# Kernel optimization log

Measured on AMD Instinct MI355X. Metric: run time of the kernel, lower is better.

The kernel has to match this reference:

```python
import jax, jax.numpy as jnp
import numpy as np

R = 16      # grid resolution per axis (G = R**3 voxels)
K = 8       # num KNN neighbors per voxel
H = 64      # num_hidden
NB = 2      # num conv blocks
EPS = 1e-5


def _conv3d(x, w, b):
    # x: [B,C,D,H,W], w: [O,I,3,3,3]
    y = jax.lax.conv_general_dilated(
        x, w, window_strides=(1, 1, 1), padding='SAME',
        dimension_numbers=('NCDHW', 'OIDHW', 'NCDHW'))
    return y + b[None, :, None, None, None]


def _bn(x):
    # training-mode BatchNorm3d statistics (no affine), per channel
    m = x.mean(axis=(0, 2, 3, 4), keepdims=True)
    v = x.var(axis=(0, 2, 3, 4), keepdims=True)
    return (x - m) * jax.lax.rsqrt(v + EPS)


def _forward(pos, x, pe_w1, pe_b1, pe_w2, pe_b2, f_w, f_b, up_w, up_b,
             conv_w, conv_b, on_g, on_b, ro_w, ro_b):
    B, N, _ = pos.shape
    # ---- Gridifier: coordinate grid over domain [-1, 1]^3 ----
    g1 = jnp.linspace(-1.0, 1.0, R, dtype=pos.dtype)
    grid = jnp.stack(jnp.meshgrid(g1, g1, g1, indexing='ij'), axis=-1).reshape(-1, 3)  # [G,3]
    # ---- brute-force KNN: points -> grid voxels (per graph) ----
    gn = jnp.sum(grid * grid, axis=-1)          # [G]
    pn = jnp.sum(pos * pos, axis=-1)            # [B,N]
    d = gn[None, :, None] + pn[:, None, :] - 2.0 * jnp.einsum('gc,bnc->bgn', grid, pos)  # [B,G,N]
    idx = jax.lax.top_k(jax.lax.stop_gradient(-d), K)[1]  # [B,G,K] nearest point indices
    b_ix = jnp.arange(B)[:, None, None]
    p_nb = pos[b_ix, idx]                       # [B,G,K,3] neighbor positions
    f_nb = x[b_ix, idx]                         # [B,G,K,Cin] neighbor features
    # ---- BipartiteConv: position-conditioned messages, mean aggregation ----
    rel = p_nb - grid[None, :, None, :]         # relative positions [B,G,K,3]
    pe = jax.nn.gelu(rel @ pe_w1 + pe_b1) @ pe_w2 + pe_b2   # position embed [B,G,K,H]
    msg = pe * (f_nb @ f_w + f_b)               # multiplicative conditioning [B,G,K,H]
    agg = msg.mean(axis=2)                      # [B,G,H]
    h = jax.nn.gelu(agg @ up_w + up_b)          # update net [B,G,H]
    # reshape(B,R,R,R,H).permute(0,4,3,2,1) -> NCDHW
    vol = h.reshape(B, R, R, R, H).transpose(0, 4, 3, 2, 1)  # [B,H,R,R,R]
    # ---- ConvNet3D: residual blocks, maxpool after block 0 ----
    for i in range(NB):
        h1 = jax.nn.relu(_bn(_conv3d(vol, conv_w[i, 0], conv_b[i, 0])))
        h2 = _bn(_conv3d(h1, conv_w[i, 1], conv_b[i, 1]))
        vol = jax.nn.relu(vol + h2)
        if i == 0:
            vol = jax.lax.reduce_window(vol, -jnp.inf, jax.lax.max,
                                        (1, 1, 2, 2, 2), (1, 1, 2, 2, 2), 'VALID')
    out = _bn(vol) * on_g[None, :, None, None, None] + on_b[None, :, None, None, None]
    # ---- mean readout pool + linear head ----
    pooled = out.mean(axis=(2, 3, 4))           # [B,H]
    return pooled @ ro_w + ro_b                 # [B,out_channels]


def setup_inputs() -> dict:
    key = jax.random.key(0)
    ks = jax.random.split(key, 10)
    B, N, Cin, OUT = 4, 4096, 3, 16
    s = 0.05
    return {
        'pos': jax.random.uniform(ks[0], (B, N, 3), jnp.float32, -1.0, 1.0),
        'x': jax.random.normal(ks[1], (B, N, Cin), jnp.float32),
        'pe_w1': jax.random.normal(ks[2], (3, H), jnp.float32) * 0.3,
        'pe_b1': jnp.zeros((H,), jnp.float32),
        'pe_w2': jax.random.normal(ks[3], (H, H), jnp.float32) * s,
        'pe_b2': jnp.zeros((H,), jnp.float32),
        'f_w': jax.random.normal(ks[4], (Cin, H), jnp.float32) * 0.3,
        'f_b': jnp.zeros((H,), jnp.float32),
        'up_w': jax.random.normal(ks[5], (H, H), jnp.float32) * s,
        'up_b': jnp.zeros((H,), jnp.float32),
        'conv_w': jax.random.normal(ks[6], (NB, 2, H, H, 3, 3, 3), jnp.float32) * s,
        'conv_b': jnp.zeros((NB, 2, H), jnp.float32),
        'on_g': jnp.ones((H,), jnp.float32),
        'on_b': jnp.zeros((H,), jnp.float32),
        'ro_w': jax.random.normal(ks[7], (H, OUT), jnp.float32) * s,
        'ro_b': jnp.zeros((OUT,), jnp.float32),
    }


def reference(pos, x, pe_w1, pe_b1, pe_w2, pe_b2, f_w, f_b, up_w, up_b,
              conv_w, conv_b, on_g, on_b, ro_w, ro_b):
    return _forward(pos, x, pe_w1, pe_b1, pe_w2, pe_b2, f_w, f_b, up_w, up_b,
                    conv_w, conv_b, on_g, on_b, ro_w, ro_b)
```

## Files before the change

### kernel.cpp

```cpp
#include <hip/hip_runtime.h>

#define ULL unsigned long long
typedef unsigned short ush;
typedef __attribute__((ext_vector_type(8))) short s8v;
typedef __attribute__((ext_vector_type(4))) float f4v;

#define BB 4
#define NP 4096
#define HH 64
#define EPSF 1e-5f

#define WH_OFF      0u
#define WL_OFF      221184u
#define WT_PER_CONV 110592u
#define IDX_OFF     442368u
#define VOL0_OFF    573440u
#define V0H_OFF     2066432u
#define V0L_OFF     2812928u
#define T1_OFF      3559424u
#define VOL1_OFF    4608000u
#define V1H_OFF     4864000u
#define V1L_OFF     4992000u
#define T3_OFF      5120000u
#define STATS_OFF   5251072u
#define CELLS_OFF   5251968u
#define SPOS_OFF    5268368u
#define MW_OFF      5333904u

#define ZN_V0   373248u
#define ZN_V1   64000u
#define ZN_ST   224u
#define ZN_ALL  (ZN_V0 + ZN_V1 + ZN_ST)

__device__ __forceinline__ ush f2bf(float f) {
  unsigned u = __float_as_uint(f);
  return (ush)((u + 0x7FFFu + ((u >> 16) & 1u)) >> 16);
}
__device__ __forceinline__ float bf2f(ush h) { return __uint_as_float(((unsigned)h) << 16); }

__device__ __forceinline__ float gelu_tanh(float v) {
  float inner = 0.7978845608028654f * (v + 0.044715f * v * v * v);
  return 0.5f * v * (1.0f + tanhf(inner));
}

__device__ __forceinline__ float lin16(int i) {
  return -1.0f + (float)i * (2.0f / 15.0f);
}

__global__ __launch_bounds__(256) void k_prep(const float* __restrict__ cw,
                                              const float* __restrict__ pw2,
                                              const float* __restrict__ upw,
                                              ush* __restrict__ wh,
                                              ush* __restrict__ wl,
                                              ush* __restrict__ mw,
                                              float* __restrict__ ws) {
  unsigned i = blockIdx.x * 256u + threadIdx.x;
  float4 z = make_float4(0.f, 0.f, 0.f, 0.f);
  if (i < ZN_V0) ((float4*)(ws + V0H_OFF))[i] = z;
  else if (i < ZN_V0 + ZN_V1) ((float4*)(ws + V1H_OFF))[i - ZN_V0] = z;
  else if (i < ZN_ALL) ((float4*)(ws + STATS_OFF))[i - ZN_V0 - ZN_V1] = z;
  if (i < 442368u) {
    unsigned conv = i / WT_PER_CONV;
    unsigned r = i - conv * WT_PER_CONV;
    unsigned co = r / 1728u;
    unsigned r2 = r - co * 1728u;
    unsigned ci = r2 / 27u;
    unsigned off = r2 - ci * 27u;
    float w = cw[i];
    ush hi = f2bf(w);
    unsigned dst = conv * WT_PER_CONV + (off * 64u + co) * 64u + ci;
    wh[dst] = hi;
    wl[dst] = f2bf(w - bf2f(hi));
  } else if (i < 450560u) {
    unsigned t = i - 442368u;
    unsigned mat = t >> 12, r = t & 4095u;
    unsigned co = r >> 6, ci = r & 63u;
    const float* src = mat ? upw : pw2;
    float w = src[ci * 64u + co];
    ush hi = f2bf(w);
    mw[mat * 8192u + co * 64u + ci] = hi;
    mw[mat * 8192u + 4096u + co * 64u + ci] = f2bf(w - bf2f(hi));
  }
}

__global__ __launch_bounds__(256) void k_bin(const float* __restrict__ pos,
                                             int* __restrict__ cellStart,
                                             float4* __restrict__ sortedPos) {
  __shared__ int cnt[4096];
  __shared__ int wsum[4];
  int tid = threadIdx.x;
  int b = blockIdx.x;
  const float* pb = pos + b * NP * 3;
  for (int i = tid; i < 4096; i += 256) cnt[i] = 0;
  __syncthreads();
#pragma unroll
  for (int t = 0; t < 16; ++t) {
    int p = t * 256 + tid;
    float px = pb[3 * p], py = pb[3 * p + 1], pz = pb[3 * p + 2];
    int c0 = (int)floorf((px + 1.0f) * 7.5f + 0.5f);
    int c1 = (int)floorf((py + 1.0f) * 7.5f + 0.5f);
    int c2 = (int)floorf((pz + 1.0f) * 7.5f + 0.5f);
    c0 = min(max(c0, 0), 15); c1 = min(max(c1, 0), 15); c2 = min(max(c2, 0), 15);
    atomicAdd(&cnt[(c0 * 16 + c1) * 16 + c2], 1);
  }
  __syncthreads();
  int base = tid * 16;
  int loc[16];
  int run = 0;
#pragma unroll
  for (int j = 0; j < 16; ++j) { loc[j] = run; run += cnt[base + j]; }
  int lane = tid & 63, wv = tid >> 6;
  int inc = run;
  for (int d = 1; d < 64; d <<= 1) {
    int o = __shfl_up(inc, d, 64);
    if (lane >= d) inc += o;
  }
  if (lane == 63) wsum[wv] = inc;
  __syncthreads();
  int woff = 0;
  for (int w = 0; w < wv; ++w) woff += wsum[w];
  int excl = woff + inc - run;
  __syncthreads();
  int stv[16];
#pragma unroll
  for (int j = 0; j < 16; ++j) {
    stv[j] = excl + loc[j];
    cellStart[b * 4097 + base + j] = stv[j];
  }
#pragma unroll
  for (int j = 0; j < 16; ++j) cnt[base + j] = stv[j];
  if (tid == 0) cellStart[b * 4097 + 4096] = NP;
  __syncthreads();
#pragma unroll
  for (int t = 0; t < 16; ++t) {
    int p = t * 256 + tid;
    float px = pb[3 * p], py = pb[3 * p + 1], pz = pb[3 * p + 2];
    int c0 = (int)floorf((px + 1.0f) * 7.5f + 0.5f);
    int c1 = (int)floorf((py + 1.0f) * 7.5f + 0.5f);
    int c2 = (int)floorf((pz + 1.0f) * 7.5f + 0.5f);
    c0 = min(max(c0, 0), 15); c1 = min(max(c1, 0), 15); c2 = min(max(c2, 0), 15);
    int slot = atomicAdd(&cnt[(c0 * 16 + c1) * 16 + c2], 1);
    sortedPos[b * 4096 + slot] = make_float4(px, py, pz, __int_as_float(p));
  }
}

__device__ __forceinline__ void ins8(ULL* kk, ULL key) {
  if (key < kk[7]) {
    kk[7] = key;
#pragma unroll
    for (int q = 7; q >= 1; --q) {
      ULL a = kk[q - 1], c = kk[q];
      bool sw = c < a;
      kk[q - 1] = sw ? c : a;
      kk[q] = sw ? a : c;
    }
  }
}
__device__ __forceinline__ void merge4(ULL* kk, int sub, ULL& win0, ULL& win1) {
#pragma unroll
  for (int r = 0; r < 8; ++r) {
    ULL m = kk[0];
    ULL o = __shfl_xor(m, 1, 64); m = (o < m) ? o : m;
    o = __shfl_xor(m, 2, 64);     m = (o < m) ? o : m;
    if (kk[0] == m) {
#pragma unroll
      for (int q = 0; q < 7; ++q) kk[q] = kk[q + 1];
      kk[7] = ~0ULL;
    }
    if (sub == (r & 3)) { if (r < 4) win0 = m; else win1 = m; }
  }
}

__device__ __forceinline__ void scan_cell(const int* __restrict__ cs,
                                          const float4* __restrict__ sp,
                                          int cell, float gx, float gy, float gz,
                                          float gn, ULL* kk) {
  int st = cs[cell], en = cs[cell + 1];
  for (int p = st; p < en; ++p) {
    float4 c = sp[p];
    float pn = c.x * c.x + c.y * c.y + c.z * c.z;
    float dt = gx * c.x + gy * c.y + gz * c.z;
    float d = (gn + pn) - 2.0f * dt;
    unsigned u = __float_as_uint(d);
    u ^= (unsigned)((int)u >> 31) | 0x80000000u;
    ins8(kk, ((ULL)u << 32) | (unsigned)__float_as_uint(c.w));
  }
}

__global__ __launch_bounds__(256) void k_knn4(const int* __restrict__ cellStart,
                                              const float4* __restrict__ sortedPos,
                                              int* __restrict__ idxo) {
  constexpr int CAP = 3072;
  __shared__ float4 pts[CAP];
  __shared__ int rst[128], rlen[128], rof[128];
  __shared__ int Tsh;
  int tid = threadIdx.x;
  int lane = tid & 63;
  int sub = tid & 3;
  int lv = tid >> 2;
  int tile = blockIdx.x;
  int b = tile >> 6;
  int t6 = tile & 63;
  int ii0 = (t6 >> 4) * 4, jj0 = ((t6 >> 2) & 3) * 4, kk0 = (t6 & 3) * 4;
  int ii = ii0 + (lv >> 4), jj = jj0 + ((lv >> 2) & 3), kkc = kk0 + (lv & 3);
  int g = (ii << 8) | (jj << 4) | kkc;
  float gx = lin16(ii), gy = lin16(jj), gz = lin16(kkc);
  float gn = gx * gx + gy * gy + gz * gz;
  const int* cs = cellStart + b * 4097;
  const float4* sp = sortedPos + b * 4096;
  int loa = max(ii0 - 3, 0), hia = min(ii0 + 6, 15);
  int lob = max(jj0 - 3, 0), hib = min(jj0 + 6, 15);
  int loc = max(kk0 - 3, 0), hic = min(kk0 + 6, 15);
  int Ra = hia - loa + 1, Rb = hib - lob + 1;
  int nrows = Ra * Rb;
  if (tid < 128) {
    int st = 0, len = 0;
    if (tid < nrows) {
      int a = loa + tid / Rb, c1 = lob + tid % Rb;
      int base = (a * 16 + c1) * 16;
      st = cs[base + loc];
      len = cs[base + hic + 1] - st;
    }
    rst[tid] = st;
    rlen[tid] = len;
  }
  __syncthreads();
  if (tid < 64) {
    int l0v = rlen[lane], l1v = rlen[lane + 64];
    int s0 = l0v;
    for (int d = 1; d < 64; d <<= 1) { int o = __shfl_up(s0, d, 64); if (lane >= d) s0 += o; }
    int tot0 = __shfl(s0, 63, 64);
    int s1 = l1v;
    for (int d = 1; d < 64; d <<= 1) { int o = __shfl_up(s1, d, 64); if (lane >= d) s1 += o; }
    int tot1 = __shfl(s1, 63, 64);
    rof[lane] = s0 - l0v;
    rof[lane + 64] = tot0 + s1 - l1v;
    if (lane == 0) Tsh = tot0 + tot1;
  }
  __syncthreads();
  int T = Tsh;
  if (T <= CAP) {
    for (int i = tid; i < T; i += 256) {
      int lo = 0, hi = nrows - 1;
      while (lo < hi) { int mid = (lo + hi + 1) >> 1; if (rof[mid] <= i) lo = mid; else hi = mid - 1; }
      pts[i] = sp[rst[lo] + (i - rof[lo])];
    }
  }
  __syncthreads();
  ULL kk[8];
#pragma unroll
  for (int q = 0; q < 8; ++q) kk[q] = ~0ULL;
  if (T <= CAP) {
    for (int i = sub; i < T; i += 4) {
      float4 c = pts[i];
      float pn = c.x * c.x + c.y * c.y + c.z * c.z;
      float dt = gx * c.x + gy * c.y + gz * c.z;
      float d = (gn + pn) - 2.0f * dt;
      unsigned u = __float_as_uint(d);
      u ^= (unsigned)((int)u >> 31) | 0x80000000u;
      ins8(kk, ((ULL)u << 32) | (unsigned)__float_as_uint(c.w));
    }
  }
  ULL win0 = ~0ULL, win1 = ~0ULL;
  merge4(kk, sub, win0, win1);
  ULL w7 = __shfl(win1, lane | 3, 64);
  int dmin = 100;
  if (loa > 0)  dmin = min(dmin, ii - loa + 1);
  if (hia < 15) dmin = min(dmin, hia + 1 - ii);
  if (lob > 0)  dmin = min(dmin, jj - lob + 1);
  if (hib < 15) dmin = min(dmin, hib + 1 - jj);
  if (loc > 0)  dmin = min(dmin, kkc - loc + 1);
  if (hic < 15) dmin = min(dmin, hic + 1 - kkc);
  float bnd = ((float)dmin - 0.5f) * (2.0f / 15.0f) - 1e-5f;
  ULL ubk = ((ULL)(__float_as_uint(bnd * bnd) | 0x80000000u)) << 32;
  if (w7 >= ubk) {
#pragma unroll
    for (int q = 0; q < 8; ++q) kk[q] = ~0ULL;
    for (int t = sub; t < 1331; t += 4) {
      int dz = t / 121, r = t - dz * 121;
      int a = ii + dz - 5, c1 = jj + (r / 11) - 5, c2 = kkc + (r % 11) - 5;
      if (((unsigned)a > 15u) | ((unsigned)c1 > 15u) | ((unsigned)c2 > 15u)) continue;
      scan_cell(cs, sp, (a * 16 + c1) * 16 + c2, gx, gy, gz, gn, kk);
    }
    merge4(kk, sub, win0, win1);
    float bnd5 = 5.5f * (2.0f / 15.0f) - 1e-5f;
    ULL ub5 = ((ULL)(__float_as_uint(bnd5 * bnd5) | 0x80000000u)) << 32;
    w7 = __shfl(win1, lane | 3, 64);
    if (w7 >= ub5) {
#pragma unroll
      for (int q = 0; q < 8; ++q) kk[q] = ~0ULL;
      for (int p = sub; p < NP; p += 4) {
        float4 c = sp[p];
        float pn = c.x * c.x + c.y * c.y + c.z * c.z;
        float dt = gx * c.x + gy * c.y + gz * c.z;
        float d = (gn + pn) - 2.0f * dt;
        unsigned u = __float_as_uint(d);
        u ^= (unsigned)((int)u >> 31) | 0x80000000u;
        ins8(kk, ((ULL)u << 32) | (unsigned)__float_as_uint(c.w));
      }
      merge4(kk, sub, win0, win1);
    }
  }
  int addr = (((b << 12) | g) << 3);
  idxo[addr + sub] = (int)(win0 & 0xFFFFFFFFULL);
  idxo[addr + sub + 4] = (int)(win1 & 0xFFFFFFFFULL);
}

__global__ __launch_bounds__(256) void k_mlp2(
    const float* __restrict__ pos, const float* __restrict__ xf,
    const float* __restrict__ w1, const float* __restrict__ b1,
    const float* __restrict__ b2v, const float* __restrict__ fw,
    const float* __restrict__ fb, const float* __restrict__ ub,
    const ush* __restrict__ w2tH, const ush* __restrict__ w2tL,
    const ush* __restrict__ uwtH, const ush* __restrict__ uwtL,
    const int* __restrict__ idx, float* __restrict__ vol0,
    ush* __restrict__ v0h, ush* __restrict__ v0l) {
  __shared__ __align__(16) ush lhH[128 * 72];
  __shared__ __align__(16) ush lhL[128 * 72];
  __shared__ __align__(16) float lfe[128 * 68];
  __shared__ __align__(16) ush agH[16 * 72];
  __shared__ __align__(16) ush agL[16 * 72];
  __shared__ float gpb[128 * 8];
  int tid = threadIdx.x, lane = tid & 63, wv = tid >> 6;
  int lm = lane & 15, quad = lane >> 4;
  int b = blockIdx.x >> 8;
  int g0 = (blockIdx.x & 255) << 4;
  s8v BH[8], BL[8], UH[2], UL[2];
#pragma unroll
  for (int n = 0; n < 4; ++n)
#pragma unroll
    for (int ks = 0; ks < 2; ++ks) {
      int o = ((n * 16 + lm) << 6) + ks * 32 + (quad << 3);
      BH[n * 2 + ks] = *(const s8v*)(w2tH + o);
      BL[n * 2 + ks] = *(const s8v*)(w2tL + o);
    }
#pragma unroll
  for (int ks = 0; ks < 2; ++ks) {
    int o = ((wv * 16 + lm) << 6) + ks * 32 + (quad << 3);
    UH[ks] = *(const s8v*)(uwtH + o);
    UL[ks] = *(const s8v*)(uwtL + o);
  }
  if (tid < 128) {
    int vi = tid >> 3, kp = tid & 7;
    int g = g0 + vi;
    int p = idx[(((b << 12) | g) << 3) + kp];
    const float* pp = pos + (b * NP + p) * 3;
    const float* xp = xf + (b * NP + p) * 3;
    gpb[tid * 8 + 0] = pp[0]; gpb[tid * 8 + 1] = pp[1]; gpb[tid * 8 + 2] = pp[2];
    gpb[tid * 8 + 3] = xp[0]; gpb[tid * 8 + 4] = xp[1]; gpb[tid * 8 + 5] = xp[2];
  }
  float w10 = w1[lane], w11 = w1[64 + lane], w12 = w1[128 + lane], b1c = b1[lane];
  float fw0 = fw[lane], fw1 = fw[64 + lane], fw2 = fw[128 + lane], fbc = fb[lane];
  float ubc = ub[wv * 16 + lm];
  float gx = lin16(g0 >> 8), gy = lin16((g0 >> 4) & 15);
  __syncthreads();
  for (int i = 0; i < 32; ++i) {
    int pair = wv * 32 + i;
    int vi = pair >> 3;
    float gz = lin16(vi);
    float r0 = gpb[pair * 8 + 0] - gx, r1 = gpb[pair * 8 + 1] - gy, r2 = gpb[pair * 8 + 2] - gz;
    float h1 = gelu_tanh(fmaf(r2, w12, fmaf(r1, w11, fmaf(r0, w10, b1c))));
    float fe = fmaf(gpb[pair * 8 + 5], fw2,
                    fmaf(gpb[pair * 8 + 4], fw1, fmaf(gpb[pair * 8 + 3], fw0, fbc)));
    ush hi = f2bf(h1);
    lhH[pair * 72 + lane] = hi;
    lhL[pair * 72 + lane] = f2bf(h1 - bf2f(hi));
    lfe[pair * 68 + lane] = fe;
  }
  f4v acc[2][4];
#pragma unroll
  for (int m = 0; m < 2; ++m)
#pragma unroll
    for (int n = 0; n < 4; ++n) acc[m][n] = (f4v){0.f, 0.f, 0.f, 0.f};
#pragma unroll
  for (int m = 0; m < 2; ++m)
#pragma unroll
    for (int ks = 0; ks < 2; ++ks) {
      int ao = (wv * 32 + m * 16 + lm) * 72 + ks * 32 + quad * 8;
      s8v Ah = *(const s8v*)&lhH[ao];
      s8v Al = *(const s8v*)&lhL[ao];
#pragma unroll
      for (int n = 0; n < 4; ++n) {
        acc[m][n] = __builtin_amdgcn_mfma_f32_16x16x32_bf16(Ah, BH[n * 2 + ks], acc[m][n], 0, 0, 0);
        acc[m][n] = __builtin_amdgcn_mfma_f32_16x16x32_bf16(Ah, BL[n * 2 + ks], acc[m][n], 0, 0, 0);
        acc[m][n] = __builtin_amdgcn_mfma_f32_16x16x32_bf16(Al, BH[n * 2 + ks], acc[m][n], 0, 0, 0);
      }
    }
  float b2c[4];
#pragma unroll
  for (int n = 0; n < 4; ++n) b2c[n] = b2v[n * 16 + lm];
#pragma unroll
  for (int m = 0; m < 2; ++m) {
    int vox = wv * 4 + m * 2 + (quad >> 1);
#pragma unroll
    for (int n = 0; n < 4; ++n) {
      float s = 0.0f;
#pragma unroll
      for (int r = 0; r < 4; ++r) {
        int pair = wv * 32 + m * 16 + quad * 4 + r;
        s += (acc[m][n][r] + b2c[n]) * lfe[pair * 68 + n * 16 + lm];
      }
      s += __shfl_xor(s, 16, 64);
      s *= 0.125f;
      if ((quad & 1) == 0) {
        ush hi = f2bf(s);
        agH[vox * 72 + n * 16 + lm] = hi;
        agL[vox * 72 + n * 16 + lm] = f2bf(s - bf2f(hi));
      }
    }
  }
  __syncthreads();
  f4v a2 = (f4v){0.f, 0.f, 0.f, 0.f};
#pragma unroll
  for (int ks = 0; ks < 2; ++ks) {
    int ao = lm * 72 + ks * 32 + quad * 8;
    s8v Ah = *(const s8v*)&agH[ao];
    s8v Al = *(const s8v*)&agL[ao];
    a2 = __builtin_amdgcn_mfma_f32_16x16x32_bf16(Ah, UH[ks], a2, 0, 0, 0);
    a2 = __builtin_amdgcn_mfma_f32_16x16x32_bf16(Ah, UL[ks], a2, 0, 0, 0);
    a2 = __builtin_amdgcn_mfma_f32_16x16x32_bf16(Al, UH[ks], a2, 0, 0, 0);
  }
  int xc = g0 >> 8, yc = (g0 >> 4) & 15;
#pragma unroll
  for (int r = 0; r < 4; ++r) {
    int vox = quad * 4 + r;
    float h = gelu_tanh(a2[r] + ubc);
    int pidx = (((b * 18 + vox + 1) * 18 + yc + 1) * 18 + xc + 1) * 64 + wv * 16 + lm;
    vol0[pidx] = h;
    ush hi = f2bf(h);
    v0h[pidx] = hi;
    v0l[pidx] = f2bf(h - bf2f(hi));
  }
}

template <int Z>
__global__ __launch_bounds__(256) void k_convm(const ush* __restrict__ vh,
                                               const ush* __restrict__ vl,
                                               const ush* __restrict__ wh,
                                               const ush* __restrict__ wl,
                                               float* __restrict__ out,
                                               float* __restrict__ stats) {
  constexpr int P = Z + 2;
  constexpr int Py = (Z == 16) ? 6 : 10;
  constexpr int Px = (Z == 16) ? 18 : 10;
  constexpr int NV = 3 * Py * Px;
  constexpr int VS = 272;
  __shared__ unsigned char slab[NV * VS];
  __shared__ float ls[64], ls2[64];
  int tid = threadIdx.x;
  int lane = tid & 63, wv = tid >> 6;
  int vbase = blockIdx.x * 64;
  int b = (Z == 16) ? (vbase >> 12) : (vbase >> 9);
  int rem = vbase & (Z * Z * Z - 1);
  int z0 = rem / (Z * Z);
  int y0 = (Z == 16) ? ((rem & 255) >> 4) : 0;
  if (tid < 64) { ls[tid] = 0.0f; ls2[tid] = 0.0f; }
  {
    constexpr int NCH = NV * 8;
    for (int i = tid; i < NCH; i += 256) {
      int v = i >> 3, c = i & 7;
      int lz = v / (Py * Px);
      int r = v - lz * (Py * Px);
      int ly = r / Px, lx = r - ly * Px;
      int g = (((b * P + z0 + lz) * P + (y0 + ly)) * P + lx) * 64 + c * 8;
      *(uint4*)(slab + v * VS + c * 16)       = *(const uint4*)(vh + g);
      *(uint4*)(slab + v * VS + 128 + c * 16) = *(const uint4*)(vl + g);
    }
  }
  __syncthreads();
  int lm = lane & 15, quad = lane >> 4;
  int co = (wv << 4) | lm;
  f4v acc[4];
#pragma unroll
  for (int m = 0; m < 4; ++m) acc[m] = (f4v){0.f, 0.f, 0.f, 0.f};
  for (int off = 0; off < 27; ++off) {
    int dz = off / 9, r9 = off - dz * 9, dy = r9 / 3, dx = r9 - dy * 3;
    const ush* bph = wh + ((off * 64 + co) << 6) + (quad << 3);
    const ush* bpl = wl + ((off * 64 + co) << 6) + (quad << 3);
#pragma unroll
    for (int ks = 0; ks < 2; ++ks) {
      s8v bhf = *(const s8v*)(bph + ks * 32);
      s8v blf = *(const s8v*)(bpl + ks * 32);
#pragma unroll
      for (int m = 0; m < 4; ++m) {
        int lyp, lxp;
        if (Z == 16) { lyp = m + dy; lxp = lm + dx; }
        else         { lyp = 2 * m + (lm >> 3) + dy; lxp = (lm & 7) + dx; }
        int sv = (dz * Py + lyp) * Px + lxp;
        const unsigned char* ap = slab + sv * VS + (quad << 4) + (ks << 6);
        s8v ahf = *(const s8v*)(ap);
        s8v alf = *(const s8v*)(ap + 128);
        acc[m] = __builtin_amdgcn_mfma_f32_16x16x32_bf16(ahf, bhf, acc[m], 0, 0, 0);
        acc[m] = __builtin_amdgcn_mfma_f32_16x16x32_bf16(ahf, blf, acc[m], 0, 0, 0);
        acc[m] = __builtin_amdgcn_mfma_f32_16x16x32_bf16(alf, bhf, acc[m], 0, 0, 0);
      }
    }
  }
  float s = 0.0f, s2 = 0.0f;
#pragma unroll
  for (int m = 0; m < 4; ++m) {
    int vx = vbase + (m << 4) + (quad << 2);
#pragma unroll
    for (int r = 0; r < 4; ++r) {
      float v = acc[m][r];
      out[(vx + r) * 64 + co] = v;
      s += v;
      s2 = fmaf(v, v, s2);
    }
  }
  atomicAdd(&ls[co], s);
  atomicAdd(&ls2[co], s2);
  __syncthreads();
  if (tid < 64) {
    atomicAdd(&stats[tid * 2], ls[tid]);
    atomicAdd(&stats[tid * 2 + 1], ls2[tid]);
  }
}

template <int Z>
__global__ __launch_bounds__(256) void k_bnrelu(const float* __restrict__ t,
                                                const float* __restrict__ stats,
                                                ush* __restrict__ outh,
                                                ush* __restrict__ outl,
                                                float inv_cnt) {
  constexpr int P = Z + 2;
  unsigned i = blockIdx.x * 256u + threadIdx.x;
  int c = i & 63;
  int vox = i >> 6;
  int x = vox % Z;
  int q = vox / Z;
  int y = q % Z;
  q /= Z;
  int z = q % Z;
  int b = q / Z;
  float m = stats[c * 2] * inv_cnt;
  float var = stats[c * 2 + 1] * inv_cnt - m * m;
  float rs = 1.0f / sqrtf(var + EPSF);
  float v = (t[i] - m) * rs;
  v = v > 0.0f ? v : 0.0f;
  int pidx = (((b * P + z + 1) * P + y + 1) * P + x + 1) * 64 + c;
  ush hi = f2bf(v);
  outh[pidx] = hi;
  outl[pidx] = f2bf(v - bf2f(hi));
}

__global__ __launch_bounds__(256) void k_residpool(const float* __restrict__ vol0,
                                                   const float* __restrict__ t2,
                                                   const float* __restrict__ stats,
                                                   float* __restrict__ vol1,
                                                   ush* __restrict__ v1h,
                                                   ush* __restrict__ v1l) {
  unsigned i = blockIdx.x * 256u + threadIdx.x;
  int c = i & 63;
  int pv = i >> 6;
  int xp = pv & 7, yp = (pv >> 3) & 7, zp = (pv >> 6) & 7, b = pv >> 9;
  float m = stats[c * 2] * (1.0f / 16384.0f);
  float var = stats[c * 2 + 1] * (1.0f / 16384.0f) - m * m;
  float rs = 1.0f / sqrtf(var + EPSF);
  float best = 0.0f;
  for (int dz = 0; dz < 2; ++dz)
    for (int dy = 0; dy < 2; ++dy)
      for (int dx = 0; dx < 2; ++dx) {
        int z = 2 * zp + dz, y = 2 * yp + dy, x = 2 * xp + dx;
        float a = vol0[(((b * 18 + z + 1) * 18 + y + 1) * 18 + x + 1) * 64 + c];
        float t = t2[(b * 4096 + z * 256 + y * 16 + x) * 64 + c];
        float u = a + (t - m) * rs;
        u = u > 0.0f ? u : 0.0f;
        best = u > best ? u : best;
      }
  int pidx = (((b * 10 + zp + 1) * 10 + yp + 1) * 10 + xp + 1) * 64 + c;
  vol1[pidx] = best;
  ush hi = f2bf(best);
  v1h[pidx] = hi;
  v1l[pidx] = f2bf(best - bf2f(hi));
}

__global__ __launch_bounds__(256) void k_resid2(const float* __restrict__ vol1,
                                                const float* __restrict__ t4,
                                                const float* __restrict__ stats,
                                                float* __restrict__ sF,
                                                float* __restrict__ sB) {
  __shared__ float ls[64], ls2[64];
  if (threadIdx.x < 64) { ls[threadIdx.x] = 0.0f; ls2[threadIdx.x] = 0.0f; }
  __syncthreads();
  unsigned i = blockIdx.x * 256u + threadIdx.x;
  int c = i & 63;
  int pv = i >> 6;
  int x = pv & 7, y = (pv >> 3) & 7, z = (pv >> 6) & 7, b = pv >> 9;
  float m = stats[c * 2] * (1.0f / 2048.0f);
  float var = stats[c * 2 + 1] * (1.0f / 2048.0f) - m * m;
  float rs = 1.0f / sqrtf(var + EPSF);
  float a = vol1[(((b * 10 + z + 1) * 10 + y + 1) * 10 + x + 1) * 64 + c];
  float u = a + (t4[i] - m) * rs;
  u = u > 0.0f ? u : 0.0f;
  atomicAdd(&ls[c], u);
  atomicAdd(&ls2[c], u * u);
  __syncthreads();
  if (threadIdx.x < 64) {
    int cc = threadIdx.x;
    atomicAdd(&sF[cc * 2], ls[cc]);
    atomicAdd(&sF[cc * 2 + 1], ls2[cc]);
    atomicAdd(&sB[b * 64 + cc], ls[cc]);
  }
}

__global__ __launch_bounds__(64) void k_final(const float* __restrict__ sF,
                                              const float* __restrict__ sB,
                                              const float* __restrict__ ong,
                                              const float* __restrict__ onb,
                                              const float* __restrict__ row,
                                              const float* __restrict__ rob,
                                              float* __restrict__ outp) {
  __shared__ float pl[4][64];
  int c = threadIdx.x;
  float m = sF[c * 2] * (1.0f / 2048.0f);
  float var = sF[c * 2 + 1] * (1.0f / 2048.0f) - m * m;
  float rs = 1.0f / sqrtf(var + EPSF);
  float gg = ong[c], bb = onb[c];
  for (int b = 0; b < 4; ++b)
    pl[b][c] = (sB[b * 64 + c] * (1.0f / 512.0f) - m) * rs * gg + bb;
  __syncthreads();
  int b = threadIdx.x >> 4, o = threadIdx.x & 15;
  float s = rob[o];
  for (int j = 0; j < 64; ++j) s = fmaf(pl[b][j], row[j * 16 + o], s);
  outp[b * 16 + o] = s;
}

extern "C" void kernel_launch(void* const* d_in, const int* in_sizes, int n_in,
                              void* d_out, int out_size, void* d_ws, size_t ws_size,
                              hipStream_t stream) {
  (void)in_sizes; (void)n_in; (void)out_size; (void)ws_size;
  const float* pos = (const float*)d_in[0];
  const float* xf  = (const float*)d_in[1];
  const float* pw1 = (const float*)d_in[2];
  const float* pb1 = (const float*)d_in[3];
  const float* pw2 = (const float*)d_in[4];
  const float* pb2 = (const float*)d_in[5];
  const float* fw  = (const float*)d_in[6];
  const float* fb  = (const float*)d_in[7];
  const float* uw  = (const float*)d_in[8];
  const float* ubp = (const float*)d_in[9];
  const float* cw  = (const float*)d_in[10];
  const float* ong = (const float*)d_in[12];
  const float* onb = (const float*)d_in[13];
  const float* row = (const float*)d_in[14];
  const float* rob = (const float*)d_in[15];

  float* ws   = (float*)d_ws;
  ush*   wh   = (ush*)(ws + WH_OFF);
  ush*   wl   = (ush*)(ws + WL_OFF);
  int*   idx  = (int*)(ws + IDX_OFF);
  float* vol0 = ws + VOL0_OFF;
  ush*   v0h  = (ush*)(ws + V0H_OFF);
  ush*   v0l  = (ush*)(ws + V0L_OFF);
  float* t1   = ws + T1_OFF;
  float* vol1 = ws + VOL1_OFF;
  ush*   v1h  = (ush*)(ws + V1H_OFF);
  ush*   v1l  = (ush*)(ws + V1L_OFF);
  float* t3   = ws + T3_OFF;
  float* sA   = ws + STATS_OFF;
  float* sF   = sA + 512;
  float* sB   = sF + 128;
  int*   cellStart = (int*)(ws + CELLS_OFF);
  float4* sortedPos = (float4*)(ws + SPOS_OFF);
  ush*   mw   = (ush*)(ws + MW_OFF);

  k_prep<<<1760, 256, 0, stream>>>(cw, pw2, uw, wh, wl, mw, ws);
  k_bin<<<4, 256, 0, stream>>>(pos, cellStart, sortedPos);
  k_knn4<<<256, 256, 0, stream>>>(cellStart, sortedPos, idx);
  k_mlp2<<<1024, 256, 0, stream>>>(pos, xf, pw1, pb1, pb2, fw, fb, ubp,
                                   mw, mw + 4096, mw + 8192, mw + 12288,
                                   idx, vol0, v0h, v0l);
  k_convm<16><<<256, 256, 0, stream>>>(v0h, v0l, wh, wl, t1, sA);
  k_bnrelu<16><<<4096, 256, 0, stream>>>(t1, sA, v0h, v0l, 1.0f / 16384.0f);
  k_convm<16><<<256, 256, 0, stream>>>(v0h, v0l, wh + WT_PER_CONV, wl + WT_PER_CONV,
                                       t1, sA + 128);
  k_residpool<<<512, 256, 0, stream>>>(vol0, t1, sA + 128, vol1, v1h, v1l);
  k_convm<8><<<32, 256, 0, stream>>>(v1h, v1l, wh + 2 * WT_PER_CONV,
                                     wl + 2 * WT_PER_CONV, t3, sA + 256);
  k_bnrelu<8><<<512, 256, 0, stream>>>(t3, sA + 256, v1h, v1l, 1.0f / 2048.0f);
  k_convm<8><<<32, 256, 0, stream>>>(v1h, v1l, wh + 3 * WT_PER_CONV,
                                     wl + 3 * WT_PER_CONV, t3, sA + 384);
  k_resid2<<<512, 256, 0, stream>>>(vol1, t3, sA + 384, sF, sB);
  k_final<<<1, 64, 0, stream>>>(sF, sB, ong, onb, row, rob, (float*)d_out);
}
```

Measured before the change: 345.7 us.

## Split KNN across 32 lanes per voxel with smaller 2x2x2 tiles

The KNN kernel now assigns 32 threads per grid voxel instead of 4 and uses 2x2x2 voxel tiles per block, so it launches 2048 blocks instead of 256. The shared candidate region shrinks to fit a 1024-point cap. The merge becomes a 5-step butterfly across 32 lanes, and the candidate loop is unrolled by two. This spreads the serial per-thread top-8 insertion work across more lanes and more blocks to raise occupancy. The cost is a longer merge, more redundant halo loads per block, and a greater chance of falling back to the slower global scan paths.

New measurement: 300.1 us. 13.2% less time.

```diff
diff --git a/kernel.cpp b/kernel.cpp
--- a/kernel.cpp
+++ b/kernel.cpp
@@ -156,19 +156,33 @@
     }
   }
 }
-__device__ __forceinline__ void merge4(ULL* kk, int sub, ULL& win0, ULL& win1) {
+__device__ __forceinline__ ULL merge32(ULL* kk, int sub) {
+  ULL win = ~0ULL;
 #pragma unroll
   for (int r = 0; r < 8; ++r) {
     ULL m = kk[0];
-    ULL o = __shfl_xor(m, 1, 64); m = (o < m) ? o : m;
-    o = __shfl_xor(m, 2, 64);     m = (o < m) ? o : m;
+#pragma unroll
+    for (int s = 1; s < 32; s <<= 1) {
+      ULL o = __shfl_xor(m, s, 64);
+      m = (o < m) ? o : m;
+    }
     if (kk[0] == m) {
 #pragma unroll
       for (int q = 0; q < 7; ++q) kk[q] = kk[q + 1];
       kk[7] = ~0ULL;
     }
-    if (sub == (r & 3)) { if (r < 4) win0 = m; else win1 = m; }
-  }
+    if (sub == r) win = m;
+  }
+  return win;
+}
+
+__device__ __forceinline__ ULL mkkey(float4 c, float gx, float gy, float gz, float gn) {
+  float pn = c.x * c.x + c.y * c.y + c.z * c.z;
+  float dt = gx * c.x + gy * c.y + gz * c.z;
+  float d = (gn + pn) - 2.0f * dt;
+  unsigned u = __float_as_uint(d);
+  u ^= (unsigned)((int)u >> 31) | 0x80000000u;
+  return ((ULL)u << 32) | (unsigned)__float_as_uint(c.w);
 }
 
 __device__ __forceinline__ void scan_cell(const int* __restrict__ cs,
@@ -176,44 +190,36 @@
                                           int cell, float gx, float gy, float gz,
                                           float gn, ULL* kk) {
   int st = cs[cell], en = cs[cell + 1];
-  for (int p = st; p < en; ++p) {
-    float4 c = sp[p];
-    float pn = c.x * c.x + c.y * c.y + c.z * c.z;
-    float dt = gx * c.x + gy * c.y + gz * c.z;
-    float d = (gn + pn) - 2.0f * dt;
-    unsigned u = __float_as_uint(d);
-    u ^= (unsigned)((int)u >> 31) | 0x80000000u;
-    ins8(kk, ((ULL)u << 32) | (unsigned)__float_as_uint(c.w));
-  }
-}
-
-__global__ __launch_bounds__(256) void k_knn4(const int* __restrict__ cellStart,
+  for (int p = st; p < en; ++p) ins8(kk, mkkey(sp[p], gx, gy, gz, gn));
+}
+
+__global__ __launch_bounds__(256) void k_knn5(const int* __restrict__ cellStart,
                                               const float4* __restrict__ sortedPos,
                                               int* __restrict__ idxo) {
-  constexpr int CAP = 3072;
+  constexpr int CAP = 1024;
   __shared__ float4 pts[CAP];
-  __shared__ int rst[128], rlen[128], rof[128];
+  __shared__ int rst[64], rlen[64], rof[64];
   __shared__ int Tsh;
   int tid = threadIdx.x;
   int lane = tid & 63;
-  int sub = tid & 3;
-  int lv = tid >> 2;
-  int tile = blockIdx.x;
-  int b = tile >> 6;
-  int t6 = tile & 63;
-  int ii0 = (t6 >> 4) * 4, jj0 = ((t6 >> 2) & 3) * 4, kk0 = (t6 & 3) * 4;
-  int ii = ii0 + (lv >> 4), jj = jj0 + ((lv >> 2) & 3), kkc = kk0 + (lv & 3);
+  int sub = tid & 31;
+  int lv = tid >> 5;
+  int blk = blockIdx.x;
+  int b = blk >> 9;
+  int t9 = blk & 511;
+  int ii0 = (t9 >> 6) * 2, jj0 = ((t9 >> 3) & 7) * 2, kk0 = (t9 & 7) * 2;
+  int ii = ii0 + (lv >> 2), jj = jj0 + ((lv >> 1) & 1), kkc = kk0 + (lv & 1);
   int g = (ii << 8) | (jj << 4) | kkc;
   float gx = lin16(ii), gy = lin16(jj), gz = lin16(kkc);
   float gn = gx * gx + gy * gy + gz * gz;
   const int* cs = cellStart + b * 4097;
   const float4* sp = sortedPos + b * 4096;
-  int loa = max(ii0 - 3, 0), hia = min(ii0 + 6, 15);
-  int lob = max(jj0 - 3, 0), hib = min(jj0 + 6, 15);
-  int loc = max(kk0 - 3, 0), hic = min(kk0 + 6, 15);
+  int loa = max(ii0 - 3, 0), hia = min(ii0 + 4, 15);
+  int lob = max(jj0 - 3, 0), hib = min(jj0 + 4, 15);
+  int loc = max(kk0 - 3, 0), hic = min(kk0 + 4, 15);
   int Ra = hia - loa + 1, Rb = hib - lob + 1;
   int nrows = Ra * Rb;
-  if (tid < 128) {
+  if (tid < 64) {
     int st = 0, len = 0;
     if (tid < nrows) {
       int a = loa + tid / Rb, c1 = lob + tid % Rb;
@@ -223,19 +229,10 @@
     }
     rst[tid] = st;
     rlen[tid] = len;
-  }
-  __syncthreads();
-  if (tid < 64) {
-    int l0v = rlen[lane], l1v = rlen[lane + 64];
-    int s0 = l0v;
+    int s0 = len;
     for (int d = 1; d < 64; d <<= 1) { int o = __shfl_up(s0, d, 64); if (lane >= d) s0 += o; }
-    int tot0 = __shfl(s0, 63, 64);
-    int s1 = l1v;
-    for (int d = 1; d < 64; d <<= 1) { int o = __shfl_up(s1, d, 64); if (lane >= d) s1 += o; }
-    int tot1 = __shfl(s1, 63, 64);
-    rof[lane] = s0 - l0v;
-    rof[lane + 64] = tot0 + s1 - l1v;
-    if (lane == 0) Tsh = tot0 + tot1;
+    rof[tid] = s0 - len;
+    if (tid == 63) Tsh = s0;
   }
   __syncthreads();
   int T = Tsh;
@@ -251,19 +248,19 @@
 #pragma unroll
   for (int q = 0; q < 8; ++q) kk[q] = ~0ULL;
   if (T <= CAP) {
-    for (int i = sub; i < T; i += 4) {
-      float4 c = pts[i];
-      float pn = c.x * c.x + c.y * c.y + c.z * c.z;
-      float dt = gx * c.x + gy * c.y + gz * c.z;
-      float d = (gn + pn) - 2.0f * dt;
-      unsigned u = __float_as_uint(d);
-      u ^= (unsigned)((int)u >> 31) | 0x80000000u;
-      ins8(kk, ((ULL)u << 32) | (unsigned)__float_as_uint(c.w));
-    }
-  }
-  ULL win0 = ~0ULL, win1 = ~0ULL;
-  merge4(kk, sub, win0, win1);
-  ULL w7 = __shfl(win1, lane | 3, 64);
+    int i = sub;
+    for (; i + 32 < T; i += 64) {
+      float4 c0 = pts[i];
+      float4 c1 = pts[i + 32];
+      ULL k0 = mkkey(c0, gx, gy, gz, gn);
+      ULL k1 = mkkey(c1, gx, gy, gz, gn);
+      ins8(kk, k0);
+      ins8(kk, k1);
+    }
+    for (; i < T; i += 32) ins8(kk, mkkey(pts[i], gx, gy, gz, gn));
+  }
+  ULL win = merge32(kk, sub);
+  ULL w7 = __shfl(win, (lane & 32) | 7, 64);
   int dmin = 100;
   if (loa > 0)  dmin = min(dmin, ii - loa + 1);
   if (hia < 15) dmin = min(dmin, hia + 1 - ii);
@@ -276,34 +273,24 @@
   if (w7 >= ubk) {
 #pragma unroll
     for (int q = 0; q < 8; ++q) kk[q] = ~0ULL;
-    for (int t = sub; t < 1331; t += 4) {
+    for (int t = sub; t < 1331; t += 32) {
       int dz = t / 121, r = t - dz * 121;
       int a = ii + dz - 5, c1 = jj + (r / 11) - 5, c2 = kkc + (r % 11) - 5;
       if (((unsigned)a > 15u) | ((unsigned)c1 > 15u) | ((unsigned)c2 > 15u)) continue;
       scan_cell(cs, sp, (a * 16 + c1) * 16 + c2, gx, gy, gz, gn, kk);
     }
-    merge4(kk, sub, win0, win1);
+    win = merge32(kk, sub);
     float bnd5 = 5.5f * (2.0f / 15.0f) - 1e-5f;
     ULL ub5 = ((ULL)(__float_as_uint(bnd5 * bnd5) | 0x80000000u)) << 32;
-    w7 = __shfl(win1, lane | 3, 64);
+    w7 = __shfl(win, (lane & 32) | 7, 64);
     if (w7 >= ub5) {
 #pragma unroll
       for (int q = 0; q < 8; ++q) kk[q] = ~0ULL;
-      for (int p = sub; p < NP; p += 4) {
-        float4 c = sp[p];
-        float pn = c.x * c.x + c.y * c.y + c.z * c.z;
-        float dt = gx * c.x + gy * c.y + gz * c.z;
-        float d = (gn + pn) - 2.0f * dt;
-        unsigned u = __float_as_uint(d);
-        u ^= (unsigned)((int)u >> 31) | 0x80000000u;
-        ins8(kk, ((ULL)u << 32) | (unsigned)__float_as_uint(c.w));
-      }
-      merge4(kk, sub, win0, win1);
-    }
-  }
-  int addr = (((b << 12) | g) << 3);
-  idxo[addr + sub] = (int)(win0 & 0xFFFFFFFFULL);
-  idxo[addr + sub + 4] = (int)(win1 & 0xFFFFFFFFULL);
+      for (int p = sub; p < NP; p += 32) ins8(kk, mkkey(sp[p], gx, gy, gz, gn));
+      win = merge32(kk, sub);
+    }
+  }
+  if (sub < 8) idxo[(((b << 12) | g) << 3) + sub] = (int)(win & 0xFFFFFFFFULL);
 }
 
 __global__ __launch_bounds__(256) void k_mlp2(
@@ -667,7 +654,7 @@
 
   k_prep<<<1760, 256, 0, stream>>>(cw, pw2, uw, wh, wl, mw, ws);
   k_bin<<<4, 256, 0, stream>>>(pos, cellStart, sortedPos);
-  k_knn4<<<256, 256, 0, stream>>>(cellStart, sortedPos, idx);
+  k_knn5<<<2048, 256, 0, stream>>>(cellStart, sortedPos, idx);
   k_mlp2<<<1024, 256, 0, stream>>>(pos, xf, pw1, pb1, pb2, fw, fb, ubp,
                                    mw, mw + 4096, mw + 8192, mw + 12288,
                                    idx, vol0, v0h, v0l);
```
